# Kernel optimization log

Measured on AMD Instinct MI355X. Metric: run time of the kernel, lower is better.

Reference implementation:

```python
import jax, jax.numpy as jnp
import numpy as np

D_MODEL = 1024
N_HEADS = 16
HEAD_DIM = D_MODEL // N_HEADS


def setup_inputs() -> dict:
    key = jax.random.key(0)
    ks = jax.random.split(key, 5)
    B, T = 2, 2048
    x = jax.random.normal(ks[0], (B, T, D_MODEL), dtype=jnp.float32)
    s_in = 1.0 / np.sqrt(D_MODEL)
    W_qkv = jax.random.normal(ks[1], (D_MODEL, 3 * D_MODEL), dtype=jnp.float32) * s_in
    b_qkv = jnp.zeros((3 * D_MODEL,), dtype=jnp.float32)
    W_out = jax.random.normal(ks[2], (D_MODEL, D_MODEL), dtype=jnp.float32) * s_in
    b_out = jnp.zeros((D_MODEL,), dtype=jnp.float32)
    gamma = jnp.ones((D_MODEL,), dtype=jnp.float32)
    beta = jnp.zeros((D_MODEL,), dtype=jnp.float32)
    return {"x": x, "W_qkv": W_qkv, "b_qkv": b_qkv, "W_out": W_out,
            "b_out": b_out, "gamma": gamma, "beta": beta}


def _layernorm(x, gamma, beta, eps=1e-5):
    mu = jnp.mean(x, axis=-1, keepdims=True)
    var = jnp.var(x, axis=-1, keepdims=True)
    return (x - mu) * jax.lax.rsqrt(var + eps) * gamma + beta


def reference(x, W_qkv, b_qkv, W_out, b_out, gamma, beta):
    B, T, D = x.shape
    residual = x
    h = _layernorm(x, gamma, beta)
    qkv = h @ W_qkv + b_qkv                      # [B, T, 3D]
    qkv = qkv.reshape(B, T, 3, N_HEADS, HEAD_DIM)
    q = jnp.transpose(qkv[:, :, 0], (0, 2, 1, 3))  # [B, H, T, hd]
    k = jnp.transpose(qkv[:, :, 1], (0, 2, 1, 3))
    v = jnp.transpose(qkv[:, :, 2], (0, 2, 1, 3))
    scale = 1.0 / np.sqrt(HEAD_DIM)
    attn = jnp.einsum("bhqd,bhkd->bhqk", q, k) * scale
    attn = jax.nn.softmax(attn, axis=-1)
    out = jnp.einsum("bhqk,bhkd->bhqd", attn, v)   # [B, H, T, hd]
    out = jnp.transpose(out, (0, 2, 1, 3)).reshape(B, T, D)
    out = out @ W_out + b_out
    return residual + out
```

## Files before the change

kernel.cpp:

```cpp
#include <hip/hip_runtime.h>
#include <hip/hip_bf16.h>


#define DINL static __device__ __forceinline__

typedef __attribute__((ext_vector_type(8))) short bf16x8;
typedef __attribute__((ext_vector_type(4))) float f32x4;

DINL float fast_exp2(float x) { return __builtin_amdgcn_exp2f(x); }

DINL unsigned short f2bf(float f) {
  __hip_bfloat16 h = __float2bfloat16(f);
  unsigned short u;
  __builtin_memcpy(&u, &h, 2);
  return u;
}

DINL unsigned int bfbits(float f) {
  unsigned int u;
  __builtin_memcpy(&u, &f, 4);
  return (u + 0x8000u) >> 16;
}

DINL void gload_lds16(const void* g, void* l) {
  __builtin_amdgcn_global_load_lds((__attribute__((address_space(1))) void*)g,
                                   (__attribute__((address_space(3))) void*)l,
                                   16, 0, 0);
}

__global__ __launch_bounds__(256)
void ln_kernel(const float* __restrict__ x, const float* __restrict__ gamma,
               const float* __restrict__ beta, unsigned short* __restrict__ h) {
  __shared__ float red[8];
  int row = blockIdx.x;
  int t = threadIdx.x;
  float4 v = reinterpret_cast<const float4*>(x + (size_t)row * 1024)[t];
  float s  = v.x + v.y + v.z + v.w;
  float sq = v.x*v.x + v.y*v.y + v.z*v.z + v.w*v.w;
#pragma unroll
  for (int off = 1; off < 64; off <<= 1) {
    s  += __shfl_xor(s, off);
    sq += __shfl_xor(sq, off);
  }
  int wid = t >> 6;
  if ((t & 63) == 0) { red[wid] = s; red[4 + wid] = sq; }
  __syncthreads();
  s  = red[0] + red[1] + red[2] + red[3];
  sq = red[4] + red[5] + red[6] + red[7];
  float mu   = s * (1.0f / 1024.0f);
  float var  = sq * (1.0f / 1024.0f) - mu * mu;
  float rstd = rsqrtf(var + 1e-5f);
  float4 g = reinterpret_cast<const float4*>(gamma)[t];
  float4 b = reinterpret_cast<const float4*>(beta)[t];
  ushort4 o;
  o.x = f2bf((v.x - mu) * rstd * g.x + b.x);
  o.y = f2bf((v.y - mu) * rstd * g.y + b.y);
  o.z = f2bf((v.z - mu) * rstd * g.z + b.z);
  o.w = f2bf((v.w - mu) * rstd * g.w + b.w);
  reinterpret_cast<ushort4*>(h + (size_t)row * 1024)[t] = o;
}

__global__ __launch_bounds__(256)
void transpose_cast_kernel(const float* __restrict__ src, unsigned short* __restrict__ dst,
                           int R, int C) {
  __shared__ float tile[32][33];
  int tx = threadIdx.x & 31, ty = threadIdx.x >> 5;
  int c0 = blockIdx.x * 32, r0 = blockIdx.y * 32;
#pragma unroll
  for (int i = 0; i < 4; i++)
    tile[ty + i * 8][tx] = src[(size_t)(r0 + ty + i * 8) * C + c0 + tx];
  __syncthreads();
#pragma unroll
  for (int i = 0; i < 4; i++) {
    int r = ty + i * 8;
    dst[(size_t)(c0 + r) * R + r0 + tx] = f2bf(tile[tx][r]);
  }
}

template <int MODE>
__global__ __launch_bounds__(256)
void gemm128(const unsigned short* __restrict__ A,
             const unsigned short* __restrict__ Bt,
             int K,
             const float* __restrict__ bias,
             unsigned short* __restrict__ qdst, unsigned short* __restrict__ kdst,
             unsigned short* __restrict__ vTdst,
             const float* __restrict__ xres, float* __restrict__ out) {
  __shared__ unsigned short As[8192];
  __shared__ unsigned short Bs[8192];
  int tid = threadIdx.x, wid = tid >> 6, lane = tid & 63;
  int l15 = lane & 15, l4 = lane >> 4;
  int brow = blockIdx.y * 128, bcol = blockIdx.x * 128;
  int wr = wid >> 1, wc = wid & 1;
  f32x4 acc[4][4] = {};

  for (int kt = 0; kt < K; kt += 64) {
    __syncthreads();
#pragma unroll
    for (int r = 0; r < 4; r++) {
      int c  = wid * 256 + r * 64;
      int cl = c + lane;
      int kb = cl >> 7, row = cl & 127;
      gload_lds16(A  + (size_t)(brow + row) * K + kt + kb * 8, As + c * 8);
      gload_lds16(Bt + (size_t)(bcol + row) * K + kt + kb * 8, Bs + c * 8);
    }
    __syncthreads();
#pragma unroll
    for (int ks = 0; ks < 2; ks++) {
      int kb = ks * 4 + l4;
      bf16x8 af[4], bfr[4];
#pragma unroll
      for (int m = 0; m < 4; m++)
        af[m] = *reinterpret_cast<const bf16x8*>(As + (kb * 128 + wr * 64 + m * 16 + l15) * 8);
#pragma unroll
      for (int n = 0; n < 4; n++)
        bfr[n] = *reinterpret_cast<const bf16x8*>(Bs + (kb * 128 + wc * 64 + n * 16 + l15) * 8);
#pragma unroll
      for (int m = 0; m < 4; m++)
#pragma unroll
        for (int n = 0; n < 4; n++)
          acc[m][n] = __builtin_amdgcn_mfma_f32_16x16x32_bf16(af[m], bfr[n], acc[m][n], 0, 0, 0);
    }
  }

  if (MODE == 0) {
    int sec = bcol >> 10;
    int secbase = sec << 10;
#pragma unroll
    for (int m = 0; m < 4; m++) {
      int row0 = brow + wr * 64 + m * 16 + l4 * 4;
      int b = row0 >> 11, t0 = row0 & 2047;
#pragma unroll
      for (int n = 0; n < 4; n++) {
        int col = (bcol & 1023) + wc * 64 + n * 16 + l15;
        float bv = bias[secbase + col];
        int hh = col >> 6, d = col & 63;
        if (sec == 2) {
          ushort4 pk;
          pk.x = f2bf(acc[m][n][0] + bv);
          pk.y = f2bf(acc[m][n][1] + bv);
          pk.z = f2bf(acc[m][n][2] + bv);
          pk.w = f2bf(acc[m][n][3] + bv);
          *reinterpret_cast<ushort4*>(vTdst + ((size_t)(b * 16 + hh) * 64 + d) * 2048 + t0) = pk;
        } else {
          unsigned short* dst = (sec == 0) ? qdst : kdst;
          float sc = (sec == 0) ? 0.125f * 1.44269504088896f : 1.0f;
#pragma unroll
          for (int j = 0; j < 4; j++)
            dst[((size_t)(b * 16 + hh) * 2048 + t0 + j) * 64 + d] = f2bf((acc[m][n][j] + bv) * sc);
        }
      }
    }
  } else {
#pragma unroll
    for (int m = 0; m < 4; m++) {
      int row0 = brow + wr * 64 + m * 16 + l4 * 4;
#pragma unroll
      for (int n = 0; n < 4; n++) {
        int col = bcol + wc * 64 + n * 16 + l15;
        float bv = bias[col];
#pragma unroll
        for (int j = 0; j < 4; j++) {
          size_t idx = (size_t)(row0 + j) * 1024 + col;
          out[idx] = acc[m][n][j] + bv + xres[idx];
        }
      }
    }
  }
}

__global__ __launch_bounds__(256, 2)
void attn_kernel(const unsigned short* __restrict__ q,
                 const unsigned short* __restrict__ kk,
                 const unsigned short* __restrict__ vT,
                 unsigned short* __restrict__ o) {
  const int T = 2048;
  __shared__ unsigned short Ks[2][4096];
  __shared__ unsigned short Ps[4][2048];
  int tid = threadIdx.x, wid = tid >> 6, lane = tid & 63;
  int l15 = lane & 15, l4 = lane >> 4;
  int swz = (l15 & 7) << 3;

  int lin = blockIdx.x;
  int rl  = (lin & 7) * 64 + (lin >> 3);
  int bx = rl & 15, bh = rl >> 4;
  int q0 = bx * 128 + wid * 32;

  const unsigned short* qh = q  + (size_t)bh * T * 64;
  const unsigned short* kh = kk + (size_t)bh * T * 64;
  const unsigned short* vh = vT + (size_t)bh * 64 * T;

  bf16x8 qf[2][2];
#pragma unroll
  for (int m = 0; m < 2; m++)
#pragma unroll
    for (int ks = 0; ks < 2; ks++)
      qf[m][ks] = *reinterpret_cast<const bf16x8*>(
          qh + (size_t)(q0 + m * 16 + l15) * 64 + ks * 32 + l4 * 8);

  f32x4 accO[2][4] = {};
  float mst[2] = {-1e30f, -1e30f}, lst[2] = {0.0f, 0.0f};

#define STAGE(buf, kv0)                                                        \
  {                                                                            \
    _Pragma("unroll") for (int r = 0; r < 2; r++) {                            \
      int c  = wid * 128 + r * 64;                                             \
      int sl = c + lane;                                                       \
      int key = sl >> 3;                                                       \
      int kb  = (sl & 7) ^ (key & 7);                                          \
      gload_lds16(kh + (size_t)((kv0) + key) * 64 + kb * 8, &Ks[buf][c * 8]);  \
    }                                                                          \
  }

  STAGE(0, 0);
  __syncthreads();
  int cur = 0;

  for (int kv0 = 0; kv0 < T; kv0 += 64) {
    bf16x8 vf[2][4];
#pragma unroll
    for (int ks = 0; ks < 2; ks++)
#pragma unroll
      for (int n = 0; n < 4; n++)
        vf[ks][n] = *reinterpret_cast<const bf16x8*>(
            vh + (size_t)(n * 16 + l15) * T + kv0 + ks * 32 + l4 * 8);

    if (kv0 + 64 < T) STAGE(cur ^ 1, kv0 + 64);

    f32x4 s[2][4] = {};
#pragma unroll
    for (int ks = 0; ks < 2; ks++) {
#pragma unroll
      for (int n = 0; n < 4; n++) {
        int slot = (n * 16 + l15) * 8 + ((ks * 4 + l4) ^ (l15 & 7));
        bf16x8 kf = *reinterpret_cast<const bf16x8*>(&Ks[cur][slot * 8]);
#pragma unroll
        for (int m = 0; m < 2; m++)
          s[m][n] = __builtin_amdgcn_mfma_f32_16x16x32_bf16(kf, qf[m][ks], s[m][n], 0, 0, 0);
      }
    }

#pragma unroll
    for (int m = 0; m < 2; m++) {
      float mx01 = fmaxf(fmaxf(s[m][0][0], s[m][0][1]), fmaxf(s[m][0][2], s[m][0][3]));
      float mx11 = fmaxf(fmaxf(s[m][1][0], s[m][1][1]), fmaxf(s[m][1][2], s[m][1][3]));
      float mx21 = fmaxf(fmaxf(s[m][2][0], s[m][2][1]), fmaxf(s[m][2][2], s[m][2][3]));
      float mx31 = fmaxf(fmaxf(s[m][3][0], s[m][3][1]), fmaxf(s[m][3][2], s[m][3][3]));
      float mx = fmaxf(fmaxf(mx01, mx11), fmaxf(mx21, mx31));
      mx = fmaxf(mx, __shfl_xor(mx, 16));
      mx = fmaxf(mx, __shfl_xor(mx, 32));
      float mnew = fmaxf(mst[m], mx);
      float a = fast_exp2(mst[m] - mnew);
      float sum = 0.0f;
#pragma unroll
      for (int n = 0; n < 4; n++) {
        unsigned int u0, u1;
#pragma unroll
        for (int j = 0; j < 4; j++) {
          float p = fast_exp2(s[m][n][j] - mnew);
          s[m][n][j] = p;
          sum += p;
        }
        u0 = bfbits(s[m][n][0]) | (bfbits(s[m][n][1]) << 16);
        u1 = bfbits(s[m][n][2]) | (bfbits(s[m][n][3]) << 16);
        *reinterpret_cast<uint2*>(
            &Ps[wid][(m * 16 + l15) * 64 + ((n * 16 + l4 * 4) ^ swz)]) =
            make_uint2(u0, u1);
      }
      sum += __shfl_xor(sum, 16);
      sum += __shfl_xor(sum, 32);
      lst[m] = lst[m] * a + sum;
      mst[m] = mnew;
#pragma unroll
      for (int n = 0; n < 4; n++)
#pragma unroll
        for (int j = 0; j < 4; j++) accO[m][n][j] *= a;
    }

#pragma unroll
    for (int ks = 0; ks < 2; ks++) {
#pragma unroll
      for (int m = 0; m < 2; m++) {
        bf16x8 pf = *reinterpret_cast<const bf16x8*>(
            &Ps[wid][(m * 16 + l15) * 64 + ((ks * 32 + l4 * 8) ^ swz)]);
#pragma unroll
        for (int n = 0; n < 4; n++)
          accO[m][n] = __builtin_amdgcn_mfma_f32_16x16x32_bf16(vf[ks][n], pf, accO[m][n], 0, 0, 0);
      }
    }

    __syncthreads();
    cur ^= 1;
  }
#undef STAGE

  int b = bh >> 4, hh = bh & 15;
#pragma unroll
  for (int m = 0; m < 2; m++) {
    float inv = 1.0f / lst[m];
    int row = q0 + m * 16 + l15;
#pragma unroll
    for (int n = 0; n < 4; n++) {
      ushort4 pk;
      pk.x = f2bf(accO[m][n][0] * inv);
      pk.y = f2bf(accO[m][n][1] * inv);
      pk.z = f2bf(accO[m][n][2] * inv);
      pk.w = f2bf(accO[m][n][3] * inv);
      *reinterpret_cast<ushort4*>(
          &o[(size_t)(b * 2048 + row) * 1024 + hh * 64 + n * 16 + l4 * 4]) = pk;
    }
  }
}

extern "C" void kernel_launch(void* const* d_in, const int* in_sizes, int n_in,
                              void* d_out, int out_size, void* d_ws, size_t ws_size,
                              hipStream_t stream) {
  const float* x     = (const float*)d_in[0];
  const float* W_qkv = (const float*)d_in[1];
  const float* b_qkv = (const float*)d_in[2];
  const float* W_out = (const float*)d_in[3];
  const float* b_out = (const float*)d_in[4];
  const float* gamma = (const float*)d_in[5];
  const float* beta  = (const float*)d_in[6];
  float* out = (float*)d_out;

  char* ws = (char*)d_ws;
  unsigned short* h     = (unsigned short*)(ws);
  unsigned short* WqkvT = (unsigned short*)(ws + (size_t)(8)  * 1024 * 1024);
  unsigned short* WoutT = (unsigned short*)(ws + (size_t)(14) * 1024 * 1024);
  unsigned short* qb    = (unsigned short*)(ws + (size_t)(16) * 1024 * 1024);
  unsigned short* kb    = (unsigned short*)(ws + (size_t)(24) * 1024 * 1024);
  unsigned short* vTb   = (unsigned short*)(ws + (size_t)(32) * 1024 * 1024);
  unsigned short* attno = (unsigned short*)(ws + (size_t)(40) * 1024 * 1024);

  ln_kernel<<<4096, 256, 0, stream>>>(x, gamma, beta, h);
  transpose_cast_kernel<<<dim3(96, 32), 256, 0, stream>>>(W_qkv, WqkvT, 1024, 3072);
  transpose_cast_kernel<<<dim3(32, 32), 256, 0, stream>>>(W_out, WoutT, 1024, 1024);
  gemm128<0><<<dim3(24, 32), 256, 0, stream>>>(h, WqkvT, 1024, b_qkv, qb, kb, vTb, nullptr, nullptr);
  attn_kernel<<<512, 256, 0, stream>>>(qb, kb, vTb, attno);
  gemm128<1><<<dim3(8, 32), 256, 0, stream>>>(attno, WoutT, 1024, b_out, nullptr, nullptr, nullptr, x, out);
}
```

Baseline: 195.6 us.

## Load K fragments directly to registers, drop LDS staging and block barrier

The attention kernel no longer stages K tiles through double-buffered shared memory. Each wave now loads its K fragments straight from global memory into registers, one tile ahead, using a register ping-pong (KA/KB) and a two-tile unrolled loop, which removes the per-tile __syncthreads. MFMA sections are wrapped in s_setprio to raise wave priority during matrix math. In exchange, all four waves now load the same K data redundantly from global/L2, and register pressure rises, which may affect occupancy at launch_bounds(256,2).

```diff
diff --git a/kernel.cpp b/kernel.cpp
--- a/kernel.cpp
+++ b/kernel.cpp
@@ -169,26 +169,118 @@
   }
 }
 
+struct AttCtx {
+  const unsigned short* kh;
+  const unsigned short* vh;
+  unsigned short* ps;
+  int l15, l4, swz;
+};
+
+template <bool DONEXT>
+DINL void att_tile(const AttCtx& c, int kv0,
+                   bf16x8 (&kc)[2][4], bf16x8 (&kn)[2][4],
+                   const bf16x8 (&qf)[2][2],
+                   f32x4 (&accO)[2][4], float (&mst)[2], float (&lst)[2]) {
+  const int T = 2048;
+  bf16x8 vf[2][4];
+#pragma unroll
+  for (int ks = 0; ks < 2; ks++)
+#pragma unroll
+    for (int n = 0; n < 4; n++)
+      vf[ks][n] = *reinterpret_cast<const bf16x8*>(
+          c.vh + (size_t)(n * 16 + c.l15) * T + kv0 + ks * 32 + c.l4 * 8);
+  if (DONEXT) {
+#pragma unroll
+    for (int ks = 0; ks < 2; ks++)
+#pragma unroll
+      for (int n = 0; n < 4; n++)
+        kn[ks][n] = *reinterpret_cast<const bf16x8*>(
+            c.kh + (size_t)(kv0 + 64 + n * 16 + c.l15) * 64 + ks * 32 + c.l4 * 8);
+  }
+
+  f32x4 s[2][4] = {};
+  __builtin_amdgcn_s_setprio(1);
+#pragma unroll
+  for (int ks = 0; ks < 2; ks++)
+#pragma unroll
+    for (int n = 0; n < 4; n++)
+#pragma unroll
+      for (int m = 0; m < 2; m++)
+        s[m][n] = __builtin_amdgcn_mfma_f32_16x16x32_bf16(kc[ks][n], qf[m][ks], s[m][n], 0, 0, 0);
+  __builtin_amdgcn_s_setprio(0);
+
+#pragma unroll
+  for (int m = 0; m < 2; m++) {
+    float mx0 = fmaxf(fmaxf(s[m][0][0], s[m][0][1]), fmaxf(s[m][0][2], s[m][0][3]));
+    float mx1 = fmaxf(fmaxf(s[m][1][0], s[m][1][1]), fmaxf(s[m][1][2], s[m][1][3]));
+    float mx2 = fmaxf(fmaxf(s[m][2][0], s[m][2][1]), fmaxf(s[m][2][2], s[m][2][3]));
+    float mx3 = fmaxf(fmaxf(s[m][3][0], s[m][3][1]), fmaxf(s[m][3][2], s[m][3][3]));
+    float mx = fmaxf(fmaxf(mx0, mx1), fmaxf(mx2, mx3));
+    mx = fmaxf(mx, __shfl_xor(mx, 16));
+    mx = fmaxf(mx, __shfl_xor(mx, 32));
+    float mnew = fmaxf(mst[m], mx);
+    float a = fast_exp2(mst[m] - mnew);
+    float sum = 0.0f;
+#pragma unroll
+    for (int n = 0; n < 4; n++) {
+#pragma unroll
+      for (int j = 0; j < 4; j++) {
+        float p = fast_exp2(s[m][n][j] - mnew);
+        s[m][n][j] = p;
+        sum += p;
+      }
+      unsigned int u0 = bfbits(s[m][n][0]) | (bfbits(s[m][n][1]) << 16);
+      unsigned int u1 = bfbits(s[m][n][2]) | (bfbits(s[m][n][3]) << 16);
+      *reinterpret_cast<uint2*>(
+          &c.ps[(m * 16 + c.l15) * 64 + ((n * 16 + c.l4 * 4) ^ c.swz)]) =
+          make_uint2(u0, u1);
+    }
+    sum += __shfl_xor(sum, 16);
+    sum += __shfl_xor(sum, 32);
+    lst[m] = lst[m] * a + sum;
+    mst[m] = mnew;
+#pragma unroll
+    for (int n = 0; n < 4; n++)
+#pragma unroll
+      for (int j = 0; j < 4; j++) accO[m][n][j] *= a;
+  }
+
+#pragma unroll
+  for (int ks = 0; ks < 2; ks++) {
+#pragma unroll
+    for (int m = 0; m < 2; m++) {
+      bf16x8 pf = *reinterpret_cast<const bf16x8*>(
+          &c.ps[(m * 16 + c.l15) * 64 + ((ks * 32 + c.l4 * 8) ^ c.swz)]);
+      __builtin_amdgcn_s_setprio(1);
+#pragma unroll
+      for (int n = 0; n < 4; n++)
+        accO[m][n] = __builtin_amdgcn_mfma_f32_16x16x32_bf16(vf[ks][n], pf, accO[m][n], 0, 0, 0);
+      __builtin_amdgcn_s_setprio(0);
+    }
+  }
+}
+
 __global__ __launch_bounds__(256, 2)
 void attn_kernel(const unsigned short* __restrict__ q,
                  const unsigned short* __restrict__ kk,
                  const unsigned short* __restrict__ vT,
                  unsigned short* __restrict__ o) {
   const int T = 2048;
-  __shared__ unsigned short Ks[2][4096];
   __shared__ unsigned short Ps[4][2048];
   int tid = threadIdx.x, wid = tid >> 6, lane = tid & 63;
   int l15 = lane & 15, l4 = lane >> 4;
-  int swz = (l15 & 7) << 3;
 
   int lin = blockIdx.x;
   int rl  = (lin & 7) * 64 + (lin >> 3);
   int bx = rl & 15, bh = rl >> 4;
   int q0 = bx * 128 + wid * 32;
 
-  const unsigned short* qh = q  + (size_t)bh * T * 64;
-  const unsigned short* kh = kk + (size_t)bh * T * 64;
-  const unsigned short* vh = vT + (size_t)bh * 64 * T;
+  AttCtx c;
+  c.kh  = kk + (size_t)bh * T * 64;
+  c.vh  = vT + (size_t)bh * 64 * T;
+  c.ps  = &Ps[wid][0];
+  c.l15 = l15; c.l4 = l4; c.swz = (l15 & 7) << 3;
+  const unsigned short* qh = q + (size_t)bh * T * 64;
 
   bf16x8 qf[2][2];
 #pragma unroll
@@ -201,98 +293,21 @@
   f32x4 accO[2][4] = {};
   float mst[2] = {-1e30f, -1e30f}, lst[2] = {0.0f, 0.0f};
 
-#define STAGE(buf, kv0)                                                        \
-  {                                                                            \
-    _Pragma("unroll") for (int r = 0; r < 2; r++) {                            \
-      int c  = wid * 128 + r * 64;                                             \
-      int sl = c + lane;                                                       \
-      int key = sl >> 3;                                                       \
-      int kb  = (sl & 7) ^ (key & 7);                                          \
-      gload_lds16(kh + (size_t)((kv0) + key) * 64 + kb * 8, &Ks[buf][c * 8]);  \
-    }                                                                          \
-  }
-
-  STAGE(0, 0);
-  __syncthreads();
-  int cur = 0;
-
-  for (int kv0 = 0; kv0 < T; kv0 += 64) {
-    bf16x8 vf[2][4];
-#pragma unroll
-    for (int ks = 0; ks < 2; ks++)
-#pragma unroll
-      for (int n = 0; n < 4; n++)
-        vf[ks][n] = *reinterpret_cast<const bf16x8*>(
-            vh + (size_t)(n * 16 + l15) * T + kv0 + ks * 32 + l4 * 8);
-
-    if (kv0 + 64 < T) STAGE(cur ^ 1, kv0 + 64);
-
-    f32x4 s[2][4] = {};
-#pragma unroll
-    for (int ks = 0; ks < 2; ks++) {
-#pragma unroll
-      for (int n = 0; n < 4; n++) {
-        int slot = (n * 16 + l15) * 8 + ((ks * 4 + l4) ^ (l15 & 7));
-        bf16x8 kf = *reinterpret_cast<const bf16x8*>(&Ks[cur][slot * 8]);
-#pragma unroll
-        for (int m = 0; m < 2; m++)
-          s[m][n] = __builtin_amdgcn_mfma_f32_16x16x32_bf16(kf, qf[m][ks], s[m][n], 0, 0, 0);
-      }
-    }
-
-#pragma unroll
-    for (int m = 0; m < 2; m++) {
-      float mx01 = fmaxf(fmaxf(s[m][0][0], s[m][0][1]), fmaxf(s[m][0][2], s[m][0][3]));
-      float mx11 = fmaxf(fmaxf(s[m][1][0], s[m][1][1]), fmaxf(s[m][1][2], s[m][1][3]));
-      float mx21 = fmaxf(fmaxf(s[m][2][0], s[m][2][1]), fmaxf(s[m][2][2], s[m][2][3]));
-      float mx31 = fmaxf(fmaxf(s[m][3][0], s[m][3][1]), fmaxf(s[m][3][2], s[m][3][3]));
-      float mx = fmaxf(fmaxf(mx01, mx11), fmaxf(mx21, mx31));
-      mx = fmaxf(mx, __shfl_xor(mx, 16));
-      mx = fmaxf(mx, __shfl_xor(mx, 32));
-      float mnew = fmaxf(mst[m], mx);
-      float a = fast_exp2(mst[m] - mnew);
-      float sum = 0.0f;
-#pragma unroll
-      for (int n = 0; n < 4; n++) {
-        unsigned int u0, u1;
-#pragma unroll
-        for (int j = 0; j < 4; j++) {
-          float p = fast_exp2(s[m][n][j] - mnew);
-          s[m][n][j] = p;
-          sum += p;
-        }
-        u0 = bfbits(s[m][n][0]) | (bfbits(s[m][n][1]) << 16);
-        u1 = bfbits(s[m][n][2]) | (bfbits(s[m][n][3]) << 16);
-        *reinterpret_cast<uint2*>(
-            &Ps[wid][(m * 16 + l15) * 64 + ((n * 16 + l4 * 4) ^ swz)]) =
-            make_uint2(u0, u1);
-      }
-      sum += __shfl_xor(sum, 16);
-      sum += __shfl_xor(sum, 32);
-      lst[m] = lst[m] * a + sum;
-      mst[m] = mnew;
-#pragma unroll
-      for (int n = 0; n < 4; n++)
-#pragma unroll
-        for (int j = 0; j < 4; j++) accO[m][n][j] *= a;
-    }
-
-#pragma unroll
-    for (int ks = 0; ks < 2; ks++) {
-#pragma unroll
-      for (int m = 0; m < 2; m++) {
-        bf16x8 pf = *reinterpret_cast<const bf16x8*>(
-            &Ps[wid][(m * 16 + l15) * 64 + ((ks * 32 + l4 * 8) ^ swz)]);
-#pragma unroll
-        for (int n = 0; n < 4; n++)
-          accO[m][n] = __builtin_amdgcn_mfma_f32_16x16x32_bf16(vf[ks][n], pf, accO[m][n], 0, 0, 0);
-      }
-    }
-
-    __syncthreads();
-    cur ^= 1;
-  }
-#undef STAGE
+  bf16x8 KA[2][4], KB[2][4];
+#pragma unroll
+  for (int ks = 0; ks < 2; ks++)
+#pragma unroll
+    for (int n = 0; n < 4; n++)
+      KA[ks][n] = *reinterpret_cast<const bf16x8*>(
+          c.kh + (size_t)(n * 16 + l15) * 64 + ks * 32 + l4 * 8);
+
+  for (int kv0 = 0; kv0 < T; kv0 += 128) {
+    att_tile<true>(c, kv0, KA, KB, qf, accO, mst, lst);
+    if (kv0 + 128 < T)
+      att_tile<true>(c, kv0 + 64, KB, KA, qf, accO, mst, lst);
+    else
+      att_tile<false>(c, kv0 + 64, KB, KA, qf, accO, mst, lst);
+  }
 
   int b = bh >> 4, hh = bh & 15;
 #pragma unroll
```

After: 225.6 us. +15.3%, slower.

## Use 128-key KV tiles with lazy softmax rescale and MFMA priority hints

Applied to the files above, without the earlier changes.

Doubles the K staging tile to 128 keys so each barrier and double-buffer swap covers two 64-key subtiles. Online softmax now skips rescaling the output accumulator when the new row max exceeds the running max by at most 11 (log2 units), which is checked wave-uniformly. Row-sum shuffles move from every iteration to a single reduction at the end. MFMA blocks are wrapped in s_setprio to favour matrix issue. The cost is more LDS per block, which may lower occupancy, and partial sums that can grow up to about 2^11 before normalisation.

```diff
diff --git a/kernel.cpp b/kernel.cpp
--- a/kernel.cpp
+++ b/kernel.cpp
@@ -175,7 +175,7 @@
                  const unsigned short* __restrict__ vT,
                  unsigned short* __restrict__ o) {
   const int T = 2048;
-  __shared__ unsigned short Ks[2][4096];
+  __shared__ unsigned short Ks[2][8192];
   __shared__ unsigned short Ps[4][2048];
   int tid = threadIdx.x, wid = tid >> 6, lane = tid & 63;
   int l15 = lane & 15, l4 = lane >> 4;
@@ -201,103 +201,135 @@
   f32x4 accO[2][4] = {};
   float mst[2] = {-1e30f, -1e30f}, lst[2] = {0.0f, 0.0f};
 
-#define STAGE(buf, kv0)                                                        \
+#define STAGE128(buf, kv0)                                                     \
   {                                                                            \
-    _Pragma("unroll") for (int r = 0; r < 2; r++) {                            \
-      int c  = wid * 128 + r * 64;                                             \
-      int sl = c + lane;                                                       \
-      int key = sl >> 3;                                                       \
-      int kb  = (sl & 7) ^ (key & 7);                                          \
+    _Pragma("unroll") for (int r = 0; r < 4; r++) {                            \
+      int c  = (wid * 4 + r) * 64;                                             \
+      int cl = c + lane;                                                       \
+      int key = cl >> 3;                                                       \
+      int kb  = (cl & 7) ^ (key & 7);                                          \
       gload_lds16(kh + (size_t)((kv0) + key) * 64 + kb * 8, &Ks[buf][c * 8]);  \
     }                                                                          \
   }
 
-  STAGE(0, 0);
+#define SUBTILE(sub, vf)                                                       \
+  {                                                                            \
+    f32x4 s[2][4] = {};                                                        \
+    __builtin_amdgcn_s_setprio(1);                                             \
+    _Pragma("unroll") for (int ks = 0; ks < 2; ks++) {                         \
+      _Pragma("unroll") for (int n = 0; n < 4; n++) {                          \
+        int kkey = (sub) * 64 + n * 16 + l15;                                  \
+        int slot = kkey * 8 + ((ks * 4 + l4) ^ (kkey & 7));                    \
+        bf16x8 kf = *reinterpret_cast<const bf16x8*>(&Ks[cur][slot * 8]);      \
+        _Pragma("unroll") for (int m = 0; m < 2; m++)                          \
+          s[m][n] = __builtin_amdgcn_mfma_f32_16x16x32_bf16(kf, qf[m][ks],     \
+                                                            s[m][n], 0, 0, 0); \
+      }                                                                        \
+    }                                                                          \
+    __builtin_amdgcn_s_setprio(0);                                             \
+    float mx[2];                                                               \
+    _Pragma("unroll") for (int m = 0; m < 2; m++) {                            \
+      float a0 = fmaxf(fmaxf(s[m][0][0], s[m][0][1]),                          \
+                       fmaxf(s[m][0][2], s[m][0][3]));                         \
+      float a1 = fmaxf(fmaxf(s[m][1][0], s[m][1][1]),                          \
+                       fmaxf(s[m][1][2], s[m][1][3]));                         \
+      float a2 = fmaxf(fmaxf(s[m][2][0], s[m][2][1]),                          \
+                       fmaxf(s[m][2][2], s[m][2][3]));                         \
+      float a3 = fmaxf(fmaxf(s[m][3][0], s[m][3][1]),                          \
+                       fmaxf(s[m][3][2], s[m][3][3]));                         \
+      float mxv = fmaxf(fmaxf(a0, a1), fmaxf(a2, a3));                         \
+      mxv = fmaxf(mxv, __shfl_xor(mxv, 16));                                   \
+      mxv = fmaxf(mxv, __shfl_xor(mxv, 32));                                   \
+      mx[m] = mxv;                                                             \
+    }                                                                          \
+    int defer = (mx[0] <= mst[0] + 11.0f) && (mx[1] <= mst[1] + 11.0f);        \
+    if (__all(defer)) {                                                        \
+      _Pragma("unroll") for (int m = 0; m < 2; m++) {                          \
+        float sum = 0.0f;                                                      \
+        _Pragma("unroll") for (int n = 0; n < 4; n++) {                        \
+          _Pragma("unroll") for (int j = 0; j < 4; j++) {                      \
+            float p = fast_exp2(s[m][n][j] - mst[m]);                          \
+            s[m][n][j] = p;                                                    \
+            sum += p;                                                          \
+          }                                                                    \
+          unsigned int u0 = bfbits(s[m][n][0]) | (bfbits(s[m][n][1]) << 16);   \
+          unsigned int u1 = bfbits(s[m][n][2]) | (bfbits(s[m][n][3]) << 16);   \
+          *reinterpret_cast<uint2*>(                                           \
+              &Ps[wid][(m * 16 + l15) * 64 + ((n * 16 + l4 * 4) ^ swz)]) =     \
+              make_uint2(u0, u1);                                              \
+        }                                                                      \
+        lst[m] += sum;                                                         \
+      }                                                                        \
+    } else {                                                                   \
+      _Pragma("unroll") for (int m = 0; m < 2; m++) {                          \
+        float mnew = fmaxf(mst[m], mx[m]);                                     \
+        float a = fast_exp2(mst[m] - mnew);                                    \
+        float sum = 0.0f;                                                      \
+        _Pragma("unroll") for (int n = 0; n < 4; n++) {                        \
+          _Pragma("unroll") for (int j = 0; j < 4; j++) {                      \
+            float p = fast_exp2(s[m][n][j] - mnew);                            \
+            s[m][n][j] = p;                                                    \
+            sum += p;                                                          \
+          }                                                                    \
+          unsigned int u0 = bfbits(s[m][n][0]) | (bfbits(s[m][n][1]) << 16);   \
+          unsigned int u1 = bfbits(s[m][n][2]) | (bfbits(s[m][n][3]) << 16);   \
+          *reinterpret_cast<uint2*>(                                           \
+              &Ps[wid][(m * 16 + l15) * 64 + ((n * 16 + l4 * 4) ^ swz)]) =     \
+              make_uint2(u0, u1);                                              \
+        }                                                                      \
+        lst[m] = lst[m] * a + sum;                                             \
+        mst[m] = mnew;                                                         \
+        _Pragma("unroll") for (int n = 0; n < 4; n++)                          \
+          _Pragma("unroll") for (int j = 0; j < 4; j++) accO[m][n][j] *= a;    \
+      }                                                                        \
+    }                                                                          \
+    _Pragma("unroll") for (int ks = 0; ks < 2; ks++) {                         \
+      _Pragma("unroll") for (int m = 0; m < 2; m++) {                          \
+        bf16x8 pf = *reinterpret_cast<const bf16x8*>(                          \
+            &Ps[wid][(m * 16 + l15) * 64 + ((ks * 32 + l4 * 8) ^ swz)]);       \
+        __builtin_amdgcn_s_setprio(1);                                         \
+        _Pragma("unroll") for (int n = 0; n < 4; n++)                          \
+          accO[m][n] = __builtin_amdgcn_mfma_f32_16x16x32_bf16(                \
+              vf[ks][n], pf, accO[m][n], 0, 0, 0);                             \
+        __builtin_amdgcn_s_setprio(0);                                         \
+      }                                                                        \
+    }                                                                          \
+  }
+
+#define LOADV(vf, kvs)                                                         \
+  {                                                                            \
+    _Pragma("unroll") for (int ks = 0; ks < 2; ks++)                           \
+      _Pragma("unroll") for (int n = 0; n < 4; n++)                            \
+        vf[ks][n] = *reinterpret_cast<const bf16x8*>(                          \
+            vh + (size_t)(n * 16 + l15) * T + (kvs) + ks * 32 + l4 * 8);       \
+  }
+
+  STAGE128(0, 0);
   __syncthreads();
   int cur = 0;
 
-  for (int kv0 = 0; kv0 < T; kv0 += 64) {
-    bf16x8 vf[2][4];
-#pragma unroll
-    for (int ks = 0; ks < 2; ks++)
-#pragma unroll
-      for (int n = 0; n < 4; n++)
-        vf[ks][n] = *reinterpret_cast<const bf16x8*>(
-            vh + (size_t)(n * 16 + l15) * T + kv0 + ks * 32 + l4 * 8);
-
-    if (kv0 + 64 < T) STAGE(cur ^ 1, kv0 + 64);
-
-    f32x4 s[2][4] = {};
-#pragma unroll
-    for (int ks = 0; ks < 2; ks++) {
-#pragma unroll
-      for (int n = 0; n < 4; n++) {
-        int slot = (n * 16 + l15) * 8 + ((ks * 4 + l4) ^ (l15 & 7));
-        bf16x8 kf = *reinterpret_cast<const bf16x8*>(&Ks[cur][slot * 8]);
-#pragma unroll
-        for (int m = 0; m < 2; m++)
-          s[m][n] = __builtin_amdgcn_mfma_f32_16x16x32_bf16(kf, qf[m][ks], s[m][n], 0, 0, 0);
-      }
-    }
-
-#pragma unroll
-    for (int m = 0; m < 2; m++) {
-      float mx01 = fmaxf(fmaxf(s[m][0][0], s[m][0][1]), fmaxf(s[m][0][2], s[m][0][3]));
-      float mx11 = fmaxf(fmaxf(s[m][1][0], s[m][1][1]), fmaxf(s[m][1][2], s[m][1][3]));
-      float mx21 = fmaxf(fmaxf(s[m][2][0], s[m][2][1]), fmaxf(s[m][2][2], s[m][2][3]));
-      float mx31 = fmaxf(fmaxf(s[m][3][0], s[m][3][1]), fmaxf(s[m][3][2], s[m][3][3]));
-      float mx = fmaxf(fmaxf(mx01, mx11), fmaxf(mx21, mx31));
-      mx = fmaxf(mx, __shfl_xor(mx, 16));
-      mx = fmaxf(mx, __shfl_xor(mx, 32));
-      float mnew = fmaxf(mst[m], mx);
-      float a = fast_exp2(mst[m] - mnew);
-      float sum = 0.0f;
-#pragma unroll
-      for (int n = 0; n < 4; n++) {
-        unsigned int u0, u1;
-#pragma unroll
-        for (int j = 0; j < 4; j++) {
-          float p = fast_exp2(s[m][n][j] - mnew);
-          s[m][n][j] = p;
-          sum += p;
-        }
-        u0 = bfbits(s[m][n][0]) | (bfbits(s[m][n][1]) << 16);
-        u1 = bfbits(s[m][n][2]) | (bfbits(s[m][n][3]) << 16);
-        *reinterpret_cast<uint2*>(
-            &Ps[wid][(m * 16 + l15) * 64 + ((n * 16 + l4 * 4) ^ swz)]) =
-            make_uint2(u0, u1);
-      }
-      sum += __shfl_xor(sum, 16);
-      sum += __shfl_xor(sum, 32);
-      lst[m] = lst[m] * a + sum;
-      mst[m] = mnew;
-#pragma unroll
-      for (int n = 0; n < 4; n++)
-#pragma unroll
-        for (int j = 0; j < 4; j++) accO[m][n][j] *= a;
-    }
-
-#pragma unroll
-    for (int ks = 0; ks < 2; ks++) {
-#pragma unroll
-      for (int m = 0; m < 2; m++) {
-        bf16x8 pf = *reinterpret_cast<const bf16x8*>(
-            &Ps[wid][(m * 16 + l15) * 64 + ((ks * 32 + l4 * 8) ^ swz)]);
-#pragma unroll
-        for (int n = 0; n < 4; n++)
-          accO[m][n] = __builtin_amdgcn_mfma_f32_16x16x32_bf16(vf[ks][n], pf, accO[m][n], 0, 0, 0);
-      }
-    }
-
+  for (int kv0 = 0; kv0 < T; kv0 += 128) {
+    bf16x8 vf0[2][4];
+    LOADV(vf0, kv0);
+    if (kv0 + 128 < T) STAGE128(cur ^ 1, kv0 + 128);
+    SUBTILE(0, vf0);
+    bf16x8 vf1[2][4];
+    LOADV(vf1, kv0 + 64);
+    SUBTILE(1, vf1);
     __syncthreads();
     cur ^= 1;
   }
-#undef STAGE
+#undef SUBTILE
+#undef LOADV
+#undef STAGE128
 
   int b = bh >> 4, hh = bh & 15;
 #pragma unroll
   for (int m = 0; m < 2; m++) {
-    float inv = 1.0f / lst[m];
+    float l = lst[m];
+    l += __shfl_xor(l, 16);
+    l += __shfl_xor(l, 32);
+    float inv = 1.0f / l;
     int row = q0 + m * 16 + l15;
 #pragma unroll
     for (int n = 0; n < 4; n++) {
```

Result: faster. 183.2 us (-6.3%).
